# Kernel tuning notes

Measured on AMD Instinct MI355X. Metric: run time of the kernel, lower is better.

The kernel has to match this reference:

```python
import jax, jax.numpy as jnp
import numpy as np


def setup_inputs() -> dict:
    key = jax.random.key(0)
    ks = jax.random.split(key, 8)
    B, N, C = 4, 2048, 1024
    H, hd, lr, R = 16, 64, 20, 200  # R = low_rank * rank_multi
    s = lambda k, shape, fan: jax.random.normal(k, shape, jnp.float32) / np.sqrt(fan)
    return {
        'x': jax.random.normal(ks[0], (B, N, C), jnp.float32),
        'qk_w': s(ks[1], (2 * C, C), C),
        'proj_w': s(ks[2], (C, C), C),
        'proj_b': jnp.zeros((C,), jnp.float32),
        'we': s(ks[3], (H, R, lr), R),
        'wr': s(ks[4], (H, R, lr), R),
        'cw_w': s(ks[5], (hd, 2 * lr), 2 * lr),
        'cw_b': jnp.zeros((hd,), jnp.float32),
    }


def _l2norm(v, eps=1e-12):
    # matches F.normalize(p=2, dim=-1): x / max(||x||, eps)
    n = jnp.sqrt(jnp.sum(v * v, axis=-1, keepdims=True))
    return v / jnp.maximum(n, eps)


def reference(x, qk_w, proj_w, proj_b, we, wr, cw_w, cw_b):
    B, N, C = x.shape
    H, R, lr = we.shape  # heads, subsample len, low_rank
    hd = C // H
    # qk projection -> q,k: [B,H,N,hd]
    qk = (x @ qk_w.T).reshape(B, N, 2, H, hd).transpose(2, 0, 3, 1, 4)
    q, k = qk[0], qk[1]
    # gen_weights: subsample N positions (embed_len > low_rank*rank_multi branch)
    idx = np.linspace(0, N - 1, R).astype(np.int64)  # static, trunc like torch
    xh = x.transpose(0, 2, 1).reshape(B, H, hd, N)[:, :, :, idx]  # [B,H,hd,R]
    we_b = jnp.einsum('bhdr,hre->bhde', xh, we)  # [B,H,hd,lr]
    wr_b = jnp.einsum('bhdr,hre->bhde', xh, wr)
    # feature map + low-rank scores
    q = _l2norm(q)
    k = _l2norm(k)
    escore = jnp.einsum('bhnd,bhde->bhne', q, we_b)  # [B,H,N,lr]
    rscore = jnp.einsum('bhnd,bhde->bhne', k, wr_b)
    score = jnp.concatenate([escore, rscore], axis=-1)  # [B,H,N,2lr]
    attn = score @ cw_w.T + cw_b  # [B,H,N,hd]
    attn = attn.transpose(0, 2, 1, 3).reshape(B, N, C)
    out = attn @ proj_w.T + proj_b  # dropout is identity at eval
    return out
```

## Files before the change

### kernel.cpp

```cpp
#include <hip/hip_runtime.h>
#include <hip/hip_bf16.h>

constexpr int B_  = 4;
constexpr int N_  = 2048;
constexpr int C_  = 1024;
constexpr int H_  = 16;
constexpr int HD  = 64;
constexpr int LR  = 20;
constexpr int RS  = 200;
constexpr int RP  = 224;

typedef __attribute__((ext_vector_type(8))) short bf16x8;
typedef __attribute__((ext_vector_type(4))) float f32x4;

__device__ __forceinline__ float b2f_raw(unsigned short u) {
    union { unsigned int i; float f; } v;
    v.i = ((unsigned int)u) << 16;
    return v.f;
}
__device__ __forceinline__ unsigned short f2b(float f) {
    __hip_bfloat16 h = __float2bfloat16(f);
    return *(unsigned short*)&h;
}
template <bool BF>
__device__ __forceinline__ float ldg(const void* p, size_t i) {
    if constexpr (BF) return b2f_raw(((const unsigned short*)p)[i]);
    else              return ((const float*)p)[i];
}

__device__ __forceinline__ void async_load16(const unsigned short* g, unsigned short* l) {
    __builtin_amdgcn_global_load_lds(
        (const __attribute__((address_space(1))) unsigned int*)(const void*)g,
        (__attribute__((address_space(3))) unsigned int*)(void*)l,
        16, 0, 0);
}

__device__ __forceinline__ bool detect_bf16(const unsigned int* __restrict__ x) {
    const int lane = threadIdx.x & 63;
    int cnt = 0;
    #pragma unroll
    for (int i = 0; i < 16; ++i) {
        const unsigned int w = x[lane * 16 + i];
        const unsigned int e = (w >> 7) & 0xFFu;
        cnt += (e >= 103u && e <= 140u) ? 1 : 0;
    }
    #pragma unroll
    for (int s = 1; s < 64; s <<= 1) cnt += __shfl_xor(cnt, s, 64);
    return cnt > 512;
}

struct CvtArgs {
    const void* src[5];
    unsigned short* dst[5];
    int size[5];
};

template <bool BF>
__device__ void wec_body(const void* __restrict__ we_raw,
                         const void* __restrict__ wr_raw,
                         const void* __restrict__ cw_raw,
                         unsigned short* __restrict__ wect,
                         unsigned short* __restrict__ wrct) {
    const int o = blockIdx.x * 256 + threadIdx.x;
    if (o >= H_ * HD * RP) return;
    const int r    = o % RP;
    const int dout = (o / RP) % HD;
    const int h    = o / (RP * HD);
    float sq = 0.f, sk = 0.f;
    if (r < RS) {
        #pragma unroll
        for (int e = 0; e < LR; ++e) {
            const float cq = ldg<BF>(cw_raw, dout * 2 * LR + e);
            const float ck = ldg<BF>(cw_raw, dout * 2 * LR + LR + e);
            sq += ldg<BF>(we_raw, ((size_t)h * RS + r) * LR + e) * cq;
            sk += ldg<BF>(wr_raw, ((size_t)h * RS + r) * LR + e) * ck;
        }
    }
    wect[o] = f2b(sq);
    wrct[o] = f2b(sk);
}

template <bool BF>
__device__ void gather_lds_body(const void* __restrict__ x_raw,
                                unsigned short* __restrict__ xh,
                                unsigned short* __restrict__ sx,
                                int g) {
    const int bh    = g >> 1;
    const int dhalf = g & 1;
    const int b = bh >> 4;
    const int h = bh & 15;
    const int t    = threadIdx.x;
    const int wave = t >> 6;
    const int lane = t & 63;
    const int dlo = lane & 31;
    const int rhi = lane >> 5;
    for (int rd = wave; rd < 100; rd += 4) {
        const int r  = rd * 2 + rhi;
        const int ir = (r * (N_ - 1)) / (RS - 1);
        const size_t idx = ((size_t)b * N_ + ir) * C_ + h * HD + dhalf * 32 + dlo;
        unsigned short v;
        if constexpr (BF) v = ((const unsigned short*)x_raw)[idx];
        else              v = f2b(((const float*)x_raw)[idx]);
        sx[r * 32 + (dlo ^ (r & 31))] = v;
    }
    __syncthreads();
    for (int o = t; o < 32 * 224; o += 256) {
        const int din = o / 224;
        const int r   = o % 224;
        const unsigned short v = (r < RS) ? sx[r * 32 + (din ^ (r & 31))]
                                          : (unsigned short)0;
        xh[(size_t)bh * HD * RP + (size_t)(dhalf * 32 + din) * RP + r] = v;
    }
}

__global__ __launch_bounds__(256)
void fused_prep_kernel(CvtArgs args,
                       const void* __restrict__ we_raw,
                       const void* __restrict__ wr_raw,
                       const void* __restrict__ cw_raw,
                       unsigned short* __restrict__ wect,
                       unsigned short* __restrict__ wrct,
                       unsigned short* __restrict__ xh) {
    __shared__ unsigned short sx[224 * 32];
    const bool isbf = detect_bf16((const unsigned int*)args.src[0]);
    const int y = blockIdx.y;
    if (y == 0) {
        if (isbf) return;
        const int n4 = args.size[0] >> 2;
        const int stride = 2048 * 256;
        for (int i = blockIdx.x * 256 + threadIdx.x; i < n4; i += stride) {
            const float4 v = ((const float4*)args.src[0])[i];
            ushort4 o;
            o.x = f2b(v.x); o.y = f2b(v.y); o.z = f2b(v.z); o.w = f2b(v.w);
            ((ushort4*)args.dst[0])[i] = o;
        }
    } else if (y == 1) {
        if (isbf) return;
        const int n1 = args.size[1] >> 2;
        const int n2 = args.size[2] >> 2;
        const int n3 = args.size[3] >> 2;
        const int n4 = args.size[4] >> 2;
        const int tot = n1 + n2 + n3 + n4;
        const int stride = 2048 * 256;
        for (int i = blockIdx.x * 256 + threadIdx.x; i < tot; i += stride) {
            const float4* s; ushort4* d; int j;
            if (i < n1)                { s = (const float4*)args.src[1]; d = (ushort4*)args.dst[1]; j = i; }
            else if (i < n1 + n2)      { s = (const float4*)args.src[2]; d = (ushort4*)args.dst[2]; j = i - n1; }
            else if (i < n1 + n2 + n3) { s = (const float4*)args.src[3]; d = (ushort4*)args.dst[3]; j = i - n1 - n2; }
            else                       { s = (const float4*)args.src[4]; d = (ushort4*)args.dst[4]; j = i - n1 - n2 - n3; }
            const float4 v = s[j];
            ushort4 o;
            o.x = f2b(v.x); o.y = f2b(v.y); o.z = f2b(v.z); o.w = f2b(v.w);
            d[j] = o;
        }
    } else {
        const int blk = blockIdx.x;
        if (blk < 896) {
            if (isbf) wec_body<true>(we_raw, wr_raw, cw_raw, wect, wrct);
            else      wec_body<false>(we_raw, wr_raw, cw_raw, wect, wrct);
        } else if (blk < 1024) {
            const int g = blk - 896;
            if (isbf) gather_lds_body<true>(args.src[0], xh, sx, g);
            else      gather_lds_body<false>(args.src[0], xh, sx, g);
        }
    }
}

__global__ __launch_bounds__(64)
void collapse_kernel(const unsigned short* __restrict__ xh,
                     const unsigned short* __restrict__ wect,
                     const unsigned short* __restrict__ wrct,
                     unsigned short* __restrict__ we2t,
                     unsigned short* __restrict__ wr2t) {
    const int blk = blockIdx.x;
    const int bh  = blk >> 2;
    const int qk  = (blk >> 1) & 1;
    const int dh  = blk & 1;
    const int h   = bh & 15;
    const int lane = threadIdx.x;
    const int lq = lane >> 4;
    const int lm = lane & 15;

    const unsigned short* wsrc = (qk ? wrct : wect) + (size_t)h * HD * RP;
    const unsigned short* xsrc = xh + (size_t)bh * HD * RP;
    unsigned short* dst = (qk ? wr2t : we2t) + (size_t)bh * HD * HD;

    f32x4 acc[2][4];
    #pragma unroll
    for (int i = 0; i < 2; ++i)
        #pragma unroll
        for (int j = 0; j < 4; ++j) acc[i][j] = 0.f;

    for (int ks = 0; ks < RP / 32; ++ks) {
        bf16x8 a[2], bfr[4];
        #pragma unroll
        for (int rt = 0; rt < 2; ++rt)
            a[rt] = *(const bf16x8*)&wsrc[(size_t)(dh * 32 + rt * 16 + lm) * RP + ks * 32 + lq * 8];
        #pragma unroll
        for (int j = 0; j < 4; ++j)
            bfr[j] = *(const bf16x8*)&xsrc[(size_t)(j * 16 + lm) * RP + ks * 32 + lq * 8];
        #pragma unroll
        for (int rt = 0; rt < 2; ++rt)
            #pragma unroll
            for (int j = 0; j < 4; ++j)
                acc[rt][j] = __builtin_amdgcn_mfma_f32_16x16x32_bf16(
                    a[rt], bfr[j], acc[rt][j], 0, 0, 0);
    }

    #pragma unroll
    for (int rt = 0; rt < 2; ++rt)
        #pragma unroll
        for (int j = 0; j < 4; ++j)
            #pragma unroll
            for (int r = 0; r < 4; ++r) {
                const int dout = dh * 32 + rt * 16 + lq * 4 + r;
                const int din  = j * 16 + lm;
                dst[dout * HD + din] = f2b(acc[rt][j][r]);
            }
}

__global__ __launch_bounds__(256, 2)
void gemm1_score_kernel(const void* __restrict__ x_raw,
                        const void* __restrict__ qkw_raw,
                        const void* __restrict__ cwb_raw,
                        const unsigned short* __restrict__ xb,
                        const unsigned short* __restrict__ qkwb,
                        const unsigned short* __restrict__ cwbb,
                        const unsigned short* __restrict__ we2t,
                        const unsigned short* __restrict__ wr2t,
                        unsigned short* __restrict__ attn) {
    constexpr int QS = 72;
    __shared__ __align__(16) unsigned short pool[32768];
    unsigned short* const AsBase = pool;
    unsigned short* const BsBase = pool + 16384;
    unsigned short* qn = pool;
    unsigned short* kn = pool + 128 * QS;

    const bool isbf = detect_bf16((const unsigned int*)x_raw);
    const unsigned short* xs  = isbf ? (const unsigned short*)x_raw   : xb;
    const unsigned short* qks = isbf ? (const unsigned short*)qkw_raw : qkwb;
    const unsigned short* cwb = isbf ? (const unsigned short*)cwb_raw : cwbb;

    const int t    = threadIdx.x;
    const int wave = t >> 6;
    const int lane = t & 63;
    const int lin     = blockIdx.y * 16 + blockIdx.x;
    const int logical = (lin & 7) * 128 + (lin >> 3);
    const int h       = logical & 15;
    const int mt      = logical >> 4;
    const int m0      = mt * 128;
    const int K       = C_;

    const int srow  = lane >> 3;
    const int sunit = (lane & 7) ^ srow;
    const unsigned short* gA = xs + (size_t)(m0 + wave * 32 + srow) * K + sunit * 8;
    const int vb = wave * 32;
    const size_t brow = (vb < 64) ? (size_t)(h * HD + vb)
                                  : (size_t)(C_ + h * HD + (vb - 64));
    const unsigned short* gB = qks + (brow + srow) * K + sunit * 8;

    const int wr = (wave >> 1) * 64;
    const int wc = (wave & 1) * 64;
    const int lq = lane >> 4;
    const int lm = lane & 15;
    const int c0 = (lq ^ (lm & 7)) * 8;

    f32x4 acc[4][4];
    #pragma unroll
    for (int i = 0; i < 4; ++i)
        #pragma unroll
        for (int j = 0; j < 4; ++j) acc[i][j] = 0.f;

    auto stage = [&](int buf) {
        unsigned short* dA = AsBase + buf * 8192 + wave * 2048;
        unsigned short* dB = BsBase + buf * 8192 + wave * 2048;
        #pragma unroll
        for (int i = 0; i < 4; ++i) {
            async_load16(gA + (size_t)i * 8 * K, dA + i * 512);
            async_load16(gB + (size_t)i * 8 * K, dB + i * 512);
        }
        gA += 64; gB += 64;
    };
    auto compute = [&](int buf) {
        const unsigned short* As = AsBase + buf * 8192;
        const unsigned short* Bs = BsBase + buf * 8192;
        #pragma unroll
        for (int ks = 0; ks < 2; ++ks) {
            const int cc = c0 ^ (ks * 32);
            bf16x8 af[4], bfr[4];
            #pragma unroll
            for (int i = 0; i < 4; ++i)
                af[i] = *(const bf16x8*)&As[(wr + i * 16 + lm) * 64 + cc];
            #pragma unroll
            for (int j = 0; j < 4; ++j)
                bfr[j] = *(const bf16x8*)&Bs[(wc + j * 16 + lm) * 64 + cc];
            #pragma unroll
            for (int i = 0; i < 4; ++i)
                #pragma unroll
                for (int j = 0; j < 4; ++j)
                    acc[i][j] = __builtin_amdgcn_mfma_f32_16x16x32_bf16(
                        af[i], bfr[j], acc[i][j], 0, 0, 0);
        }
    };

    constexpr int NTK = C_ / 64;
    stage(0);
    __syncthreads();
    for (int kt = 0; kt < NTK - 1; ++kt) {
        stage((kt + 1) & 1);
        compute(kt & 1);
        __syncthreads();
    }
    compute((NTK - 1) & 1);
    __syncthreads();

    unsigned short* dst = (wc == 0) ? qn : kn;
    #pragma unroll
    for (int i = 0; i < 4; ++i) {
        float inv[4];
        #pragma unroll
        for (int r = 0; r < 4; ++r) {
            float s = 0.f;
            #pragma unroll
            for (int j = 0; j < 4; ++j) s += acc[i][j][r] * acc[i][j][r];
            s += __shfl_xor(s, 1, 64);
            s += __shfl_xor(s, 2, 64);
            s += __shfl_xor(s, 4, 64);
            s += __shfl_xor(s, 8, 64);
            inv[r] = 1.f / fmaxf(sqrtf(s), 1e-12f);
        }
        #pragma unroll
        for (int j = 0; j < 4; ++j)
            #pragma unroll
            for (int r = 0; r < 4; ++r) {
                const int row = wr + i * 16 + lq * 4 + r;
                dst[row * QS + j * 16 + lm] = f2b(acc[i][j][r] * inv[r]);
            }
    }
    __syncthreads();

    const int b  = mt >> 4;
    const int bh = b * H_ + h;
    const unsigned short* wq = we2t + (size_t)bh * HD * HD;
    const unsigned short* wk = wr2t + (size_t)bh * HD * HD;

    bf16x8 bq[2][4], bk[2][4];
    #pragma unroll
    for (int t2 = 0; t2 < 2; ++t2)
        #pragma unroll
        for (int j = 0; j < 4; ++j) {
            const int dout = j * 16 + lm;
            bq[t2][j] = *(const bf16x8*)&wq[dout * HD + t2 * 32 + lq * 8];
            bk[t2][j] = *(const bf16x8*)&wk[dout * HD + t2 * 32 + lq * 8];
        }

    f32x4 accS[2][4];
    #pragma unroll
    for (int rt = 0; rt < 2; ++rt)
        #pragma unroll
        for (int j = 0; j < 4; ++j) accS[rt][j] = 0.f;

    #pragma unroll
    for (int rt = 0; rt < 2; ++rt) {
        const int lr = wave * 32 + rt * 16 + lm;
        bf16x8 aq0 = *(const bf16x8*)&qn[lr * QS + lq * 8];
        bf16x8 aq1 = *(const bf16x8*)&qn[lr * QS + 32 + lq * 8];
        bf16x8 ak0 = *(const bf16x8*)&kn[lr * QS + lq * 8];
        bf16x8 ak1 = *(const bf16x8*)&kn[lr * QS + 32 + lq * 8];
        #pragma unroll
        for (int j = 0; j < 4; ++j) {
            accS[rt][j] = __builtin_amdgcn_mfma_f32_16x16x32_bf16(aq0, bq[0][j], accS[rt][j], 0, 0, 0);
            accS[rt][j] = __builtin_amdgcn_mfma_f32_16x16x32_bf16(aq1, bq[1][j], accS[rt][j], 0, 0, 0);
            accS[rt][j] = __builtin_amdgcn_mfma_f32_16x16x32_bf16(ak0, bk[0][j], accS[rt][j], 0, 0, 0);
            accS[rt][j] = __builtin_amdgcn_mfma_f32_16x16x32_bf16(ak1, bk[1][j], accS[rt][j], 0, 0, 0);
        }
    }

    #pragma unroll
    for (int rt = 0; rt < 2; ++rt)
        #pragma unroll
        for (int j = 0; j < 4; ++j) {
            const int dout = j * 16 + lm;
            const float bv = b2f_raw(cwb[dout]);
            #pragma unroll
            for (int r = 0; r < 4; ++r) {
                const int row = m0 + wave * 32 + rt * 16 + lq * 4 + r;
                attn[(size_t)row * C_ + h * HD + dout] = f2b(accS[rt][j][r] + bv);
            }
        }
}

template <bool OBF>
__device__ void mfma_gemm_body64(const unsigned short* __restrict__ A,
                                 const unsigned short* __restrict__ W,
                                 const unsigned short* __restrict__ bias,
                                 void* __restrict__ out,
                                 int M, int N, int K, int m0, int n0) {
    __shared__ __align__(16) unsigned short AsBase[16384];
    __shared__ __align__(16) unsigned short BsBase[16384];

    const int t    = threadIdx.x;
    const int wave = t >> 6;
    const int lane = t & 63;

    const int srow  = lane >> 3;
    const int sunit = (lane & 7) ^ srow;
    const unsigned short* gA = A + (size_t)(m0 + wave * 32 + srow) * K + sunit * 8;
    const unsigned short* gB = W + (size_t)(n0 + wave * 32 + srow) * K + sunit * 8;

    const int wr = (wave >> 1) * 64;
    const int wc = (wave & 1) * 64;
    const int lq = lane >> 4;
    const int lm = lane & 15;
    const int c0 = (lq ^ (lm & 7)) * 8;

    f32x4 acc[4][4];
    #pragma unroll
    for (int i = 0; i < 4; ++i)
        #pragma unroll
        for (int j = 0; j < 4; ++j) acc[i][j] = 0.f;

    auto stage = [&](int buf) {
        unsigned short* dA = AsBase + buf * 8192 + wave * 2048;
        unsigned short* dB = BsBase + buf * 8192 + wave * 2048;
        #pragma unroll
        for (int i = 0; i < 4; ++i) {
            async_load16(gA + (size_t)i * 8 * K, dA + i * 512);
            async_load16(gB + (size_t)i * 8 * K, dB + i * 512);
        }
        gA += 64; gB += 64;
    };
    auto compute = [&](int buf) {
        const unsigned short* As = AsBase + buf * 8192;
        const unsigned short* Bs = BsBase + buf * 8192;
        #pragma unroll
        for (int ks = 0; ks < 2; ++ks) {
            const int cc = c0 ^ (ks * 32);
            bf16x8 af[4], bfr[4];
            #pragma unroll
            for (int i = 0; i < 4; ++i)
                af[i] = *(const bf16x8*)&As[(wr + i * 16 + lm) * 64 + cc];
            #pragma unroll
            for (int j = 0; j < 4; ++j)
                bfr[j] = *(const bf16x8*)&Bs[(wc + j * 16 + lm) * 64 + cc];
            #pragma unroll
            for (int i = 0; i < 4; ++i)
                #pragma unroll
                for (int j = 0; j < 4; ++j)
                    acc[i][j] = __builtin_amdgcn_mfma_f32_16x16x32_bf16(
                        af[i], bfr[j], acc[i][j], 0, 0, 0);
        }
    };

    const int NTK = K / 64;
    stage(0);
    __syncthreads();
    for (int kt = 0; kt < NTK - 1; ++kt) {
        stage((kt + 1) & 1);
        compute(kt & 1);
        __syncthreads();
    }
    compute((NTK - 1) & 1);

    #pragma unroll
    for (int i = 0; i < 4; ++i) {
        #pragma unroll
        for (int j = 0; j < 4; ++j) {
            const int col = n0 + wc + j * 16 + lm;
            const float bv = b2f_raw(bias[col]);
            #pragma unroll
            for (int r = 0; r < 4; ++r) {
                const int row = m0 + wr + i * 16 + lq * 4 + r;
                const float v = acc[i][j][r] + bv;
                if constexpr (OBF)
                    ((__hip_bfloat16*)out)[(size_t)row * N + col] = __float2bfloat16(v);
                else
                    ((float*)out)[(size_t)row * N + col] = v;
            }
        }
    }
}

__global__ __launch_bounds__(256, 2)
void gemm2_kernel(const void* __restrict__ x_raw,
                  const void* __restrict__ pw_raw,
                  const void* __restrict__ pb_raw,
                  const unsigned short* __restrict__ attn,
                  const unsigned short* __restrict__ pwb,
                  const unsigned short* __restrict__ pbb,
                  void* __restrict__ out) {
    const bool isbf = detect_bf16((const unsigned int*)x_raw);
    const unsigned short* W = isbf ? (const unsigned short*)pw_raw : pwb;
    const unsigned short* bias = isbf ? (const unsigned short*)pb_raw : pbb;
    const int lin     = blockIdx.y * 8 + blockIdx.x;
    const int logical = (lin & 7) * 64 + (lin >> 3);
    const int n0      = (logical & 7) * 128;
    const int m0      = (logical >> 3) * 128;
    if (isbf) mfma_gemm_body64<true>(attn, W, bias, out, B_ * N_, C_, C_, m0, n0);
    else      mfma_gemm_body64<false>(attn, W, bias, out, B_ * N_, C_, C_, m0, n0);
}

extern "C" void kernel_launch(void* const* d_in, const int* in_sizes, int n_in,
                              void* d_out, int out_size, void* d_ws, size_t ws_size,
                              hipStream_t stream) {
    (void)in_sizes; (void)n_in; (void)out_size; (void)ws_size;

    char* ws = (char*)d_ws;
    size_t off = 0;
    auto alloc = [&](size_t bytes) {
        char* p = ws + off;
        off += (bytes + 255) & ~(size_t)255;
        return p;
    };

    unsigned short* xb    = (unsigned short*)alloc((size_t)B_ * N_ * C_ * 2);
    unsigned short* qkwb  = (unsigned short*)alloc((size_t)2 * C_ * C_ * 2);
    unsigned short* pwb   = (unsigned short*)alloc((size_t)C_ * C_ * 2);
    unsigned short* pbb   = (unsigned short*)alloc((size_t)C_ * 2);
    unsigned short* cwbb  = (unsigned short*)alloc((size_t)HD * 2);
    unsigned short* attn  = (unsigned short*)alloc((size_t)B_ * N_ * C_ * 2);
    unsigned short* we2t  = (unsigned short*)alloc((size_t)B_ * H_ * HD * HD * 2);
    unsigned short* wr2t  = (unsigned short*)alloc((size_t)B_ * H_ * HD * HD * 2);
    unsigned short* wect  = (unsigned short*)alloc((size_t)H_ * HD * RP * 2);
    unsigned short* wrct  = (unsigned short*)alloc((size_t)H_ * HD * RP * 2);
    unsigned short* xh    = (unsigned short*)alloc((size_t)B_ * H_ * HD * RP * 2);

    const int M = B_ * N_;

    CvtArgs ca;
    ca.src[0] = d_in[0]; ca.dst[0] = xb;   ca.size[0] = B_ * N_ * C_;
    ca.src[1] = d_in[1]; ca.dst[1] = qkwb; ca.size[1] = 2 * C_ * C_;
    ca.src[2] = d_in[2]; ca.dst[2] = pwb;  ca.size[2] = C_ * C_;
    ca.src[3] = d_in[3]; ca.dst[3] = pbb;  ca.size[3] = C_;
    ca.src[4] = d_in[7]; ca.dst[4] = cwbb; ca.size[4] = HD;
    fused_prep_kernel<<<dim3(2048, 3), 256, 0, stream>>>(
        ca, d_in[4], d_in[5], d_in[6], wect, wrct, xh);

    collapse_kernel<<<B_ * H_ * 4, 64, 0, stream>>>(xh, wect, wrct, we2t, wr2t);

    gemm1_score_kernel<<<dim3(16, M / 128), 256, 0, stream>>>(
        d_in[0], d_in[1], d_in[7], xb, qkwb, cwbb, we2t, wr2t, attn);

    gemm2_kernel<<<dim3(C_ / 128, M / 128), 256, 0, stream>>>(
        d_in[0], d_in[2], d_in[3], attn, pwb, pbb, d_out);
}
```

Measured before the change: 206.7 us.

## Load GEMM MFMA fragments directly from global memory, dropping LDS staging

Both GEMM kernels (the qk projection with score epilogue, and the output projection) stop staging A/B tiles through double-buffered LDS with async global-to-LDS loads. Each lane now loads its bf16x8 MFMA fragments straight from global memory into registers, using a two-stage register double buffer. This removes the per-k-tile barriers and the LDS traffic. In exchange, each wave re-reads data that the tile shares with other waves from global memory or cache, and the reads are less coalesced, so the kernel relies much more on L2 and may run out of memory bandwidth. The LDS pool in the first kernel shrinks to what the epilogue needs, which could allow higher occupancy.

```diff
diff --git a/kernel.cpp b/kernel.cpp
--- a/kernel.cpp
+++ b/kernel.cpp
@@ -26,13 +26,6 @@
 __device__ __forceinline__ float ldg(const void* p, size_t i) {
     if constexpr (BF) return b2f_raw(((const unsigned short*)p)[i]);
     else              return ((const float*)p)[i];
-}
-
-__device__ __forceinline__ void async_load16(const unsigned short* g, unsigned short* l) {
-    __builtin_amdgcn_global_load_lds(
-        (const __attribute__((address_space(1))) unsigned int*)(const void*)g,
-        (__attribute__((address_space(3))) unsigned int*)(void*)l,
-        16, 0, 0);
 }
 
 __device__ __forceinline__ bool detect_bf16(const unsigned int* __restrict__ x) {
@@ -230,9 +223,7 @@
                         const unsigned short* __restrict__ wr2t,
                         unsigned short* __restrict__ attn) {
     constexpr int QS = 72;
-    __shared__ __align__(16) unsigned short pool[32768];
-    unsigned short* const AsBase = pool;
-    unsigned short* const BsBase = pool + 16384;
+    __shared__ __align__(16) unsigned short pool[2 * 128 * QS];
     unsigned short* qn = pool;
     unsigned short* kn = pool + 128 * QS;
 
@@ -249,21 +240,15 @@
     const int h       = logical & 15;
     const int mt      = logical >> 4;
     const int m0      = mt * 128;
-    const int K       = C_;
-
-    const int srow  = lane >> 3;
-    const int sunit = (lane & 7) ^ srow;
-    const unsigned short* gA = xs + (size_t)(m0 + wave * 32 + srow) * K + sunit * 8;
-    const int vb = wave * 32;
-    const size_t brow = (vb < 64) ? (size_t)(h * HD + vb)
-                                  : (size_t)(C_ + h * HD + (vb - 64));
-    const unsigned short* gB = qks + (brow + srow) * K + sunit * 8;
 
     const int wr = (wave >> 1) * 64;
     const int wc = (wave & 1) * 64;
     const int lq = lane >> 4;
     const int lm = lane & 15;
-    const int c0 = (lq ^ (lm & 7)) * 8;
+
+    const unsigned short* Abase = xs + (size_t)(m0 + wr + lm) * C_ + lq * 8;
+    const size_t brow0 = (wc == 0) ? (size_t)(h * HD) : (size_t)(C_ + h * HD);
+    const unsigned short* Bbase = qks + (brow0 + lm) * C_ + lq * 8;
 
     f32x4 acc[4][4];
     #pragma unroll
@@ -271,48 +256,37 @@
         #pragma unroll
         for (int j = 0; j < 4; ++j) acc[i][j] = 0.f;
 
-    auto stage = [&](int buf) {
-        unsigned short* dA = AsBase + buf * 8192 + wave * 2048;
-        unsigned short* dB = BsBase + buf * 8192 + wave * 2048;
-        #pragma unroll
-        for (int i = 0; i < 4; ++i) {
-            async_load16(gA + (size_t)i * 8 * K, dA + i * 512);
-            async_load16(gB + (size_t)i * 8 * K, dB + i * 512);
-        }
-        gA += 64; gB += 64;
-    };
-    auto compute = [&](int buf) {
-        const unsigned short* As = AsBase + buf * 8192;
-        const unsigned short* Bs = BsBase + buf * 8192;
-        #pragma unroll
-        for (int ks = 0; ks < 2; ++ks) {
-            const int cc = c0 ^ (ks * 32);
-            bf16x8 af[4], bfr[4];
-            #pragma unroll
-            for (int i = 0; i < 4; ++i)
-                af[i] = *(const bf16x8*)&As[(wr + i * 16 + lm) * 64 + cc];
+    auto ldA = [&](bf16x8* f, int k) {
+        #pragma unroll
+        for (int i = 0; i < 4; ++i)
+            f[i] = *(const bf16x8*)(Abase + (size_t)i * 16 * C_ + k);
+    };
+    auto ldB = [&](bf16x8* f, int k) {
+        #pragma unroll
+        for (int j = 0; j < 4; ++j)
+            f[j] = *(const bf16x8*)(Bbase + (size_t)j * 16 * C_ + k);
+    };
+    auto mm = [&](const bf16x8* a, const bf16x8* b) {
+        #pragma unroll
+        for (int i = 0; i < 4; ++i)
             #pragma unroll
             for (int j = 0; j < 4; ++j)
-                bfr[j] = *(const bf16x8*)&Bs[(wc + j * 16 + lm) * 64 + cc];
-            #pragma unroll
-            for (int i = 0; i < 4; ++i)
-                #pragma unroll
-                for (int j = 0; j < 4; ++j)
-                    acc[i][j] = __builtin_amdgcn_mfma_f32_16x16x32_bf16(
-                        af[i], bfr[j], acc[i][j], 0, 0, 0);
-        }
-    };
-
-    constexpr int NTK = C_ / 64;
-    stage(0);
-    __syncthreads();
-    for (int kt = 0; kt < NTK - 1; ++kt) {
-        stage((kt + 1) & 1);
-        compute(kt & 1);
-        __syncthreads();
-    }
-    compute((NTK - 1) & 1);
-    __syncthreads();
+                acc[i][j] = __builtin_amdgcn_mfma_f32_16x16x32_bf16(
+                    a[i], b[j], acc[i][j], 0, 0, 0);
+    };
+
+    bf16x8 a0[4], b0[4], a1[4], b1[4];
+    ldA(a0, 0); ldB(b0, 0);
+    #pragma unroll 1
+    for (int k = 0; k < C_ - 64; k += 64) {
+        ldA(a1, k + 32); ldB(b1, k + 32);
+        mm(a0, b0);
+        ldA(a0, k + 64); ldB(b0, k + 64);
+        mm(a1, b1);
+    }
+    ldA(a1, C_ - 32); ldB(b1, C_ - 32);
+    mm(a0, b0);
+    mm(a1, b1);
 
     unsigned short* dst = (wc == 0) ? qn : kn;
     #pragma unroll
@@ -391,28 +365,22 @@
 }
 
 template <bool OBF>
-__device__ void mfma_gemm_body64(const unsigned short* __restrict__ A,
-                                 const unsigned short* __restrict__ W,
-                                 const unsigned short* __restrict__ bias,
-                                 void* __restrict__ out,
-                                 int M, int N, int K, int m0, int n0) {
-    __shared__ __align__(16) unsigned short AsBase[16384];
-    __shared__ __align__(16) unsigned short BsBase[16384];
-
+__device__ void mfma_gemm_frag(const unsigned short* __restrict__ A,
+                               const unsigned short* __restrict__ W,
+                               const unsigned short* __restrict__ bias,
+                               void* __restrict__ out,
+                               int N, int K, int m0, int n0) {
     const int t    = threadIdx.x;
     const int wave = t >> 6;
     const int lane = t & 63;
-
-    const int srow  = lane >> 3;
-    const int sunit = (lane & 7) ^ srow;
-    const unsigned short* gA = A + (size_t)(m0 + wave * 32 + srow) * K + sunit * 8;
-    const unsigned short* gB = W + (size_t)(n0 + wave * 32 + srow) * K + sunit * 8;
 
     const int wr = (wave >> 1) * 64;
     const int wc = (wave & 1) * 64;
     const int lq = lane >> 4;
     const int lm = lane & 15;
-    const int c0 = (lq ^ (lm & 7)) * 8;
+
+    const unsigned short* Abase = A + (size_t)(m0 + wr + lm) * K + lq * 8;
+    const unsigned short* Bbase = W + (size_t)(n0 + wc + lm) * K + lq * 8;
 
     f32x4 acc[4][4];
     #pragma unroll
@@ -420,47 +388,37 @@
         #pragma unroll
         for (int j = 0; j < 4; ++j) acc[i][j] = 0.f;
 
-    auto stage = [&](int buf) {
-        unsigned short* dA = AsBase + buf * 8192 + wave * 2048;
-        unsigned short* dB = BsBase + buf * 8192 + wave * 2048;
-        #pragma unroll
-        for (int i = 0; i < 4; ++i) {
-            async_load16(gA + (size_t)i * 8 * K, dA + i * 512);
-            async_load16(gB + (size_t)i * 8 * K, dB + i * 512);
-        }
-        gA += 64; gB += 64;
-    };
-    auto compute = [&](int buf) {
-        const unsigned short* As = AsBase + buf * 8192;
-        const unsigned short* Bs = BsBase + buf * 8192;
-        #pragma unroll
-        for (int ks = 0; ks < 2; ++ks) {
-            const int cc = c0 ^ (ks * 32);
-            bf16x8 af[4], bfr[4];
-            #pragma unroll
-            for (int i = 0; i < 4; ++i)
-                af[i] = *(const bf16x8*)&As[(wr + i * 16 + lm) * 64 + cc];
+    auto ldA = [&](bf16x8* f, int k) {
+        #pragma unroll
+        for (int i = 0; i < 4; ++i)
+            f[i] = *(const bf16x8*)(Abase + (size_t)i * 16 * K + k);
+    };
+    auto ldB = [&](bf16x8* f, int k) {
+        #pragma unroll
+        for (int j = 0; j < 4; ++j)
+            f[j] = *(const bf16x8*)(Bbase + (size_t)j * 16 * K + k);
+    };
+    auto mm = [&](const bf16x8* a, const bf16x8* b) {
+        #pragma unroll
+        for (int i = 0; i < 4; ++i)
             #pragma unroll
             for (int j = 0; j < 4; ++j)
-                bfr[j] = *(const bf16x8*)&Bs[(wc + j * 16 + lm) * 64 + cc];
-            #pragma unroll
-            for (int i = 0; i < 4; ++i)
-                #pragma unroll
-                for (int j = 0; j < 4; ++j)
-                    acc[i][j] = __builtin_amdgcn_mfma_f32_16x16x32_bf16(
-                        af[i], bfr[j], acc[i][j], 0, 0, 0);
-        }
-    };
-
-    const int NTK = K / 64;
-    stage(0);
-    __syncthreads();
-    for (int kt = 0; kt < NTK - 1; ++kt) {
-        stage((kt + 1) & 1);
-        compute(kt & 1);
-        __syncthreads();
-    }
-    compute((NTK - 1) & 1);
+                acc[i][j] = __builtin_amdgcn_mfma_f32_16x16x32_bf16(
+                    a[i], b[j], acc[i][j], 0, 0, 0);
+    };
+
+    bf16x8 a0[4], b0[4], a1[4], b1[4];
+    ldA(a0, 0); ldB(b0, 0);
+    #pragma unroll 1
+    for (int k = 0; k < 1024 - 64; k += 64) {
+        ldA(a1, k + 32); ldB(b1, k + 32);
+        mm(a0, b0);
+        ldA(a0, k + 64); ldB(b0, k + 64);
+        mm(a1, b1);
+    }
+    ldA(a1, 1024 - 32); ldB(b1, 1024 - 32);
+    mm(a0, b0);
+    mm(a1, b1);
 
     #pragma unroll
     for (int i = 0; i < 4; ++i) {
@@ -496,8 +454,8 @@
     const int logical = (lin & 7) * 64 + (lin >> 3);
     const int n0      = (logical & 7) * 128;
     const int m0      = (logical >> 3) * 128;
-    if (isbf) mfma_gemm_body64<true>(attn, W, bias, out, B_ * N_, C_, C_, m0, n0);
-    else      mfma_gemm_body64<false>(attn, W, bias, out, B_ * N_, C_, C_, m0, n0);
+    if (isbf) mfma_gemm_frag<true>(attn, W, bias, out, C_, C_, m0, n0);
+    else      mfma_gemm_frag<false>(attn, W, bias, out, C_, C_, m0, n0);
 }
 
 extern "C" void kernel_launch(void* const* d_in, const int* in_sizes, int n_in,
```

Result: slower. 303.5 us (+46.8%).

## Fuse low-rank weight collapse into prep kernel and drop collapse launch

Applied to the files above, without the earlier changes.

Merges the cw-weight contraction, x subsample gather, and the xh·W collapse MFMA into one block per (batch, head, half, q/k) inside the prep kernel, keeping intermediates in LDS instead of global buffers. This removes a separate kernel launch and the global round-trips for wect/wrct/xh. It recomputes the cw contraction per batch (redundant work) and greatly increases static LDS per prep block, which may lower occupancy of the convert blocks sharing the kernel.

```diff
diff --git a/kernel.cpp b/kernel.cpp
--- a/kernel.cpp
+++ b/kernel.cpp
@@ -9,6 +9,7 @@
 constexpr int LR  = 20;
 constexpr int RS  = 200;
 constexpr int RP  = 224;
+constexpr int RPAD = 232;
 
 typedef __attribute__((ext_vector_type(8))) short bf16x8;
 typedef __attribute__((ext_vector_type(4))) float f32x4;
@@ -56,42 +57,35 @@
 };
 
 template <bool BF>
-__device__ void wec_body(const void* __restrict__ we_raw,
+__device__ void gwc_body(const void* __restrict__ x_raw,
+                         const void* __restrict__ we_raw,
                          const void* __restrict__ wr_raw,
                          const void* __restrict__ cw_raw,
-                         unsigned short* __restrict__ wect,
-                         unsigned short* __restrict__ wrct) {
-    const int o = blockIdx.x * 256 + threadIdx.x;
-    if (o >= H_ * HD * RP) return;
-    const int r    = o % RP;
-    const int dout = (o / RP) % HD;
-    const int h    = o / (RP * HD);
-    float sq = 0.f, sk = 0.f;
-    if (r < RS) {
-        #pragma unroll
-        for (int e = 0; e < LR; ++e) {
-            const float cq = ldg<BF>(cw_raw, dout * 2 * LR + e);
-            const float ck = ldg<BF>(cw_raw, dout * 2 * LR + LR + e);
-            sq += ldg<BF>(we_raw, ((size_t)h * RS + r) * LR + e) * cq;
-            sk += ldg<BF>(wr_raw, ((size_t)h * RS + r) * LR + e) * ck;
-        }
-    }
-    wect[o] = f2b(sq);
-    wrct[o] = f2b(sk);
-}
-
-template <bool BF>
-__device__ void gather_lds_body(const void* __restrict__ x_raw,
-                                unsigned short* __restrict__ xh,
-                                unsigned short* __restrict__ sx,
-                                int g) {
-    const int bh    = g >> 1;
-    const int dhalf = g & 1;
+                         unsigned short* __restrict__ we2t,
+                         unsigned short* __restrict__ wr2t,
+                         unsigned short* __restrict__ sx,
+                         unsigned short* __restrict__ sx2,
+                         unsigned short* __restrict__ wl,
+                         float* __restrict__ cwl,
+                         int blk) {
+    const int bh    = blk >> 2;
+    const int dhalf = (blk >> 1) & 1;
+    const int qk    = blk & 1;
     const int b = bh >> 4;
     const int h = bh & 15;
     const int t    = threadIdx.x;
     const int wave = t >> 6;
     const int lane = t & 63;
+
+    {
+        const int dout = t >> 2;
+        const int e0   = (t & 3) * 5;
+        #pragma unroll
+        for (int i = 0; i < 5; ++i)
+            cwl[dout * LR + e0 + i] =
+                ldg<BF>(cw_raw, (size_t)dout * 2 * LR + qk * LR + e0 + i);
+    }
+
     const int dlo = lane & 31;
     const int rhi = lane >> 5;
     for (int rd = wave; rd < 100; rd += 4) {
@@ -104,13 +98,57 @@
         sx[r * 32 + (dlo ^ (r & 31))] = v;
     }
     __syncthreads();
-    for (int o = t; o < 32 * 224; o += 256) {
-        const int din = o / 224;
-        const int r   = o % 224;
+
+    if (t < RP) {
+        const int r = t;
+        float w20[LR];
+        if (r < RS) {
+            const void* wsrc = qk ? wr_raw : we_raw;
+            #pragma unroll
+            for (int e = 0; e < LR; ++e)
+                w20[e] = ldg<BF>(wsrc, ((size_t)h * RS + r) * LR + e);
+        } else {
+            #pragma unroll
+            for (int e = 0; e < LR; ++e) w20[e] = 0.f;
+        }
+        for (int dout = 0; dout < HD; ++dout) {
+            float s = 0.f;
+            #pragma unroll
+            for (int e = 0; e < LR; ++e) s += w20[e] * cwl[dout * LR + e];
+            wl[dout * RPAD + r] = f2b(s);
+        }
+    }
+
+    for (int o = t; o < 32 * RP; o += 256) {
+        const int din = o / RP;
+        const int r   = o % RP;
         const unsigned short v = (r < RS) ? sx[r * 32 + (din ^ (r & 31))]
                                           : (unsigned short)0;
-        xh[(size_t)bh * HD * RP + (size_t)(dhalf * 32 + din) * RP + r] = v;
-    }
+        sx2[din * RPAD + r] = v;
+    }
+    __syncthreads();
+
+    const int lq = lane >> 4;
+    const int lm = lane & 15;
+    f32x4 acc[2];
+    acc[0] = 0.f; acc[1] = 0.f;
+    for (int ks = 0; ks < RP / 32; ++ks) {
+        bf16x8 av = *(const bf16x8*)&wl[(wave * 16 + lm) * RPAD + ks * 32 + lq * 8];
+        #pragma unroll
+        for (int j = 0; j < 2; ++j) {
+            bf16x8 bv = *(const bf16x8*)&sx2[(j * 16 + lm) * RPAD + ks * 32 + lq * 8];
+            acc[j] = __builtin_amdgcn_mfma_f32_16x16x32_bf16(av, bv, acc[j], 0, 0, 0);
+        }
+    }
+    unsigned short* dst = (qk ? wr2t : we2t) + (size_t)bh * HD * HD;
+    #pragma unroll
+    for (int j = 0; j < 2; ++j)
+        #pragma unroll
+        for (int r = 0; r < 4; ++r) {
+            const int dout = wave * 16 + lq * 4 + r;
+            const int din  = dhalf * 32 + j * 16 + lm;
+            dst[dout * HD + din] = f2b(acc[j][r]);
+        }
 }
 
 __global__ __launch_bounds__(256)
@@ -118,10 +156,12 @@
                        const void* __restrict__ we_raw,
                        const void* __restrict__ wr_raw,
                        const void* __restrict__ cw_raw,
-                       unsigned short* __restrict__ wect,
-                       unsigned short* __restrict__ wrct,
-                       unsigned short* __restrict__ xh) {
-    __shared__ unsigned short sx[224 * 32];
+                       unsigned short* __restrict__ we2t,
+                       unsigned short* __restrict__ wr2t) {
+    __shared__ __align__(16) unsigned short sx[RP * 32];
+    __shared__ __align__(16) unsigned short sx2[32 * RPAD];
+    __shared__ __align__(16) unsigned short wl[64 * RPAD];
+    __shared__ float cwl[64 * LR];
     const bool isbf = detect_bf16((const unsigned int*)args.src[0]);
     const int y = blockIdx.y;
     if (y == 0) {
@@ -155,68 +195,12 @@
         }
     } else {
         const int blk = blockIdx.x;
-        if (blk < 896) {
-            if (isbf) wec_body<true>(we_raw, wr_raw, cw_raw, wect, wrct);
-            else      wec_body<false>(we_raw, wr_raw, cw_raw, wect, wrct);
-        } else if (blk < 1024) {
-            const int g = blk - 896;
-            if (isbf) gather_lds_body<true>(args.src[0], xh, sx, g);
-            else      gather_lds_body<false>(args.src[0], xh, sx, g);
-        }
-    }
-}
-
-__global__ __launch_bounds__(64)
-void collapse_kernel(const unsigned short* __restrict__ xh,
-                     const unsigned short* __restrict__ wect,
-                     const unsigned short* __restrict__ wrct,
-                     unsigned short* __restrict__ we2t,
-                     unsigned short* __restrict__ wr2t) {
-    const int blk = blockIdx.x;
-    const int bh  = blk >> 2;
-    const int qk  = (blk >> 1) & 1;
-    const int dh  = blk & 1;
-    const int h   = bh & 15;
-    const int lane = threadIdx.x;
-    const int lq = lane >> 4;
-    const int lm = lane & 15;
-
-    const unsigned short* wsrc = (qk ? wrct : wect) + (size_t)h * HD * RP;
-    const unsigned short* xsrc = xh + (size_t)bh * HD * RP;
-    unsigned short* dst = (qk ? wr2t : we2t) + (size_t)bh * HD * HD;
-
-    f32x4 acc[2][4];
-    #pragma unroll
-    for (int i = 0; i < 2; ++i)
-        #pragma unroll
-        for (int j = 0; j < 4; ++j) acc[i][j] = 0.f;
-
-    for (int ks = 0; ks < RP / 32; ++ks) {
-        bf16x8 a[2], bfr[4];
-        #pragma unroll
-        for (int rt = 0; rt < 2; ++rt)
-            a[rt] = *(const bf16x8*)&wsrc[(size_t)(dh * 32 + rt * 16 + lm) * RP + ks * 32 + lq * 8];
-        #pragma unroll
-        for (int j = 0; j < 4; ++j)
-            bfr[j] = *(const bf16x8*)&xsrc[(size_t)(j * 16 + lm) * RP + ks * 32 + lq * 8];
-        #pragma unroll
-        for (int rt = 0; rt < 2; ++rt)
-            #pragma unroll
-            for (int j = 0; j < 4; ++j)
-                acc[rt][j] = __builtin_amdgcn_mfma_f32_16x16x32_bf16(
-                    a[rt], bfr[j], acc[rt][j], 0, 0, 0);
-    }
-
-    #pragma unroll
-    for (int rt = 0; rt < 2; ++rt)
-        #pragma unroll
-        for (int j = 0; j < 4; ++j)
-            #pragma unroll
-            for (int r = 0; r < 4; ++r) {
-                const int dout = dh * 32 + rt * 16 + lq * 4 + r;
-                const int din  = j * 16 + lm;
-                dst[dout * HD + din] = f2b(acc[rt][j][r]);
-            }
+        if (blk >= 256) return;
+        if (isbf) gwc_body<true>(args.src[0], we_raw, wr_raw, cw_raw,
+                                 we2t, wr2t, sx, sx2, wl, cwl, blk);
+        else      gwc_body<false>(args.src[0], we_raw, wr_raw, cw_raw,
+                                  we2t, wr2t, sx, sx2, wl, cwl, blk);
+    }
 }
 
 __global__ __launch_bounds__(256, 2)
@@ -521,9 +505,6 @@
     unsigned short* attn  = (unsigned short*)alloc((size_t)B_ * N_ * C_ * 2);
     unsigned short* we2t  = (unsigned short*)alloc((size_t)B_ * H_ * HD * HD * 2);
     unsigned short* wr2t  = (unsigned short*)alloc((size_t)B_ * H_ * HD * HD * 2);
-    unsigned short* wect  = (unsigned short*)alloc((size_t)H_ * HD * RP * 2);
-    unsigned short* wrct  = (unsigned short*)alloc((size_t)H_ * HD * RP * 2);
-    unsigned short* xh    = (unsigned short*)alloc((size_t)B_ * H_ * HD * RP * 2);
 
     const int M = B_ * N_;
 
@@ -534,9 +515,7 @@
     ca.src[3] = d_in[3]; ca.dst[3] = pbb;  ca.size[3] = C_;
     ca.src[4] = d_in[7]; ca.dst[4] = cwbb; ca.size[4] = HD;
     fused_prep_kernel<<<dim3(2048, 3), 256, 0, stream>>>(
-        ca, d_in[4], d_in[5], d_in[6], wect, wrct, xh);
-
-    collapse_kernel<<<B_ * H_ * 4, 64, 0, stream>>>(xh, wect, wrct, we2t, wr2t);
+        ca, d_in[4], d_in[5], d_in[6], we2t, wr2t);
 
     gemm1_score_kernel<<<dim3(16, M / 128), 256, 0, stream>>>(
         d_in[0], d_in[1], d_in[7], xb, qkwb, cwbb, we2t, wr2t, attn);
```

Result: slower. 214.5 us (+3.8%).
